# Kernel tuning notes

Hardware: AMD Instinct MI355X
Metric: run time of the kernel (lower is better)

The kernel has to match this reference:

```python
import math
import jax, jax.numpy as jnp
import numpy as np

DEGREE = 8
N = 8388608


def setup_inputs() -> dict:
    key = jax.random.key(0)
    k1, k2 = jax.random.split(key)
    X = jax.random.normal(k1, (N,), dtype=jnp.float32)
    w = jax.random.normal(k2, (DEGREE,), dtype=jnp.float32) * 0.1
    b = jnp.zeros((1,), dtype=jnp.float32)
    return {"X": X, "w": w, "b": b}


def reference(X, w, b):
    # exponents 0..degree-1; broadcast power expansion over the batch
    exponents = jnp.arange(DEGREE, dtype=jnp.float32)              # [D]
    gamma_factors = jnp.asarray(
        [1.0 / math.gamma(i + 1) for i in range(DEGREE)], dtype=jnp.float32
    )                                                              # [D]
    poly = jnp.power(X[:, None], exponents[None, :])               # [N, D]
    poly = poly * gamma_factors                                    # [N, D]
    return poly @ w + b                                            # [N]
```

## Files before the change

### kernel.cpp

```cpp
#include <hip/hip_runtime.h>
#include <hip/hip_bf16.h>


__global__ __launch_bounds__(256) void PolyModel_poly_kernel(
    const float* __restrict__ X,
    const float* __restrict__ w,
    const float* __restrict__ b,
    float* __restrict__ out,
    int n4)
{
    const float c0 = w[0] + b[0];
    const float c1 = w[1];
    const float c2 = w[2] * 0.5f;
    const float c3 = w[3] * (1.0f / 6.0f);
    const float c4 = w[4] * (1.0f / 24.0f);
    const float c5 = w[5] * (1.0f / 120.0f);
    const float c6 = w[6] * (1.0f / 720.0f);
    const float c7 = w[7] * (1.0f / 5040.0f);

    const int stride = gridDim.x * blockDim.x;
    for (int i = blockIdx.x * blockDim.x + threadIdx.x; i < n4; i += stride) {
        float4 x = reinterpret_cast<const float4*>(X)[i];
        float4 r;
        r.x = fmaf(fmaf(fmaf(fmaf(fmaf(fmaf(fmaf(c7, x.x, c6), x.x, c5), x.x, c4), x.x, c3), x.x, c2), x.x, c1), x.x, c0);
        r.y = fmaf(fmaf(fmaf(fmaf(fmaf(fmaf(fmaf(c7, x.y, c6), x.y, c5), x.y, c4), x.y, c3), x.y, c2), x.y, c1), x.y, c0);
        r.z = fmaf(fmaf(fmaf(fmaf(fmaf(fmaf(fmaf(c7, x.z, c6), x.z, c5), x.z, c4), x.z, c3), x.z, c2), x.z, c1), x.z, c0);
        r.w = fmaf(fmaf(fmaf(fmaf(fmaf(fmaf(fmaf(c7, x.w, c6), x.w, c5), x.w, c4), x.w, c3), x.w, c2), x.w, c1), x.w, c0);
        reinterpret_cast<float4*>(out)[i] = r;
    }
}

extern "C" void kernel_launch(void* const* d_in, const int* in_sizes, int n_in,
                              void* d_out, int out_size, void* d_ws, size_t ws_size,
                              hipStream_t stream) {
    const float* X = (const float*)d_in[0];
    const float* w = (const float*)d_in[1];
    const float* b = (const float*)d_in[2];
    float* out = (float*)d_out;

    const int n = in_sizes[0];
    const int n4 = n / 4;

    const int block = 256;
    int grid = (n4 + block - 1) / block;
    if (grid > 2048) grid = 2048;

    PolyModel_poly_kernel<<<grid, block, 0, stream>>>(X, w, b, out, n4);
}
```

Baseline: 15.76 us.

## Add exact-fit unrolled kernel with nontemporal loads and stores

Adds a fast-path kernel used when the size divides evenly. Each thread issues four independent float4 nontemporal loads up front, then computes and writes with nontemporal stores. The grid is sized exactly to the work instead of a capped grid-stride loop. This aims to raise memory-level parallelism, drop loop overhead and avoid polluting the cache on a streaming workload, at the cost of a second code path.

```diff
diff --git a/kernel.cpp b/kernel.cpp
--- a/kernel.cpp
+++ b/kernel.cpp
@@ -2,11 +2,62 @@
 #include <hip/hip_bf16.h>
 
 
-__global__ __launch_bounds__(256) void PolyModel_poly_kernel(
-    const float* __restrict__ X,
+typedef float f32x4 __attribute__((ext_vector_type(4)));
+
+#define UNROLL 4
+
+__device__ __forceinline__ float horner8(float x, float c0, float c1, float c2,
+                                         float c3, float c4, float c5, float c6,
+                                         float c7) {
+    float r = fmaf(c7, x, c6);
+    r = fmaf(r, x, c5);
+    r = fmaf(r, x, c4);
+    r = fmaf(r, x, c3);
+    r = fmaf(r, x, c2);
+    r = fmaf(r, x, c1);
+    r = fmaf(r, x, c0);
+    return r;
+}
+
+__global__ __launch_bounds__(256) void PolyModel_poly_fast(
+    const f32x4* __restrict__ X,
     const float* __restrict__ w,
     const float* __restrict__ b,
-    float* __restrict__ out,
+    f32x4* __restrict__ out,
+    int stride)
+{
+    const float c0 = w[0] + b[0];
+    const float c1 = w[1];
+    const float c2 = w[2] * 0.5f;
+    const float c3 = w[3] * (1.0f / 6.0f);
+    const float c4 = w[4] * (1.0f / 24.0f);
+    const float c5 = w[5] * (1.0f / 120.0f);
+    const float c6 = w[6] * (1.0f / 720.0f);
+    const float c7 = w[7] * (1.0f / 5040.0f);
+
+    const int tid = blockIdx.x * blockDim.x + threadIdx.x;
+
+    f32x4 x[UNROLL];
+#pragma unroll
+    for (int u = 0; u < UNROLL; ++u)
+        x[u] = __builtin_nontemporal_load(&X[tid + u * stride]);
+
+#pragma unroll
+    for (int u = 0; u < UNROLL; ++u) {
+        f32x4 r;
+        r.x = horner8(x[u].x, c0, c1, c2, c3, c4, c5, c6, c7);
+        r.y = horner8(x[u].y, c0, c1, c2, c3, c4, c5, c6, c7);
+        r.z = horner8(x[u].z, c0, c1, c2, c3, c4, c5, c6, c7);
+        r.w = horner8(x[u].w, c0, c1, c2, c3, c4, c5, c6, c7);
+        __builtin_nontemporal_store(r, &out[tid + u * stride]);
+    }
+}
+
+__global__ __launch_bounds__(256) void PolyModel_poly_generic(
+    const f32x4* __restrict__ X,
+    const float* __restrict__ w,
+    const float* __restrict__ b,
+    f32x4* __restrict__ out,
     int n4)
 {
     const float c0 = w[0] + b[0];
@@ -20,30 +71,36 @@
 
     const int stride = gridDim.x * blockDim.x;
     for (int i = blockIdx.x * blockDim.x + threadIdx.x; i < n4; i += stride) {
-        float4 x = reinterpret_cast<const float4*>(X)[i];
-        float4 r;
-        r.x = fmaf(fmaf(fmaf(fmaf(fmaf(fmaf(fmaf(c7, x.x, c6), x.x, c5), x.x, c4), x.x, c3), x.x, c2), x.x, c1), x.x, c0);
-        r.y = fmaf(fmaf(fmaf(fmaf(fmaf(fmaf(fmaf(c7, x.y, c6), x.y, c5), x.y, c4), x.y, c3), x.y, c2), x.y, c1), x.y, c0);
-        r.z = fmaf(fmaf(fmaf(fmaf(fmaf(fmaf(fmaf(c7, x.z, c6), x.z, c5), x.z, c4), x.z, c3), x.z, c2), x.z, c1), x.z, c0);
-        r.w = fmaf(fmaf(fmaf(fmaf(fmaf(fmaf(fmaf(c7, x.w, c6), x.w, c5), x.w, c4), x.w, c3), x.w, c2), x.w, c1), x.w, c0);
-        reinterpret_cast<float4*>(out)[i] = r;
+        f32x4 x = X[i];
+        f32x4 r;
+        r.x = horner8(x.x, c0, c1, c2, c3, c4, c5, c6, c7);
+        r.y = horner8(x.y, c0, c1, c2, c3, c4, c5, c6, c7);
+        r.z = horner8(x.z, c0, c1, c2, c3, c4, c5, c6, c7);
+        r.w = horner8(x.w, c0, c1, c2, c3, c4, c5, c6, c7);
+        out[i] = r;
     }
 }
 
 extern "C" void kernel_launch(void* const* d_in, const int* in_sizes, int n_in,
                               void* d_out, int out_size, void* d_ws, size_t ws_size,
                               hipStream_t stream) {
-    const float* X = (const float*)d_in[0];
+    const f32x4* X = (const f32x4*)d_in[0];
     const float* w = (const float*)d_in[1];
     const float* b = (const float*)d_in[2];
-    float* out = (float*)d_out;
+    f32x4* out = (f32x4*)d_out;
 
     const int n = in_sizes[0];
     const int n4 = n / 4;
 
     const int block = 256;
-    int grid = (n4 + block - 1) / block;
-    if (grid > 2048) grid = 2048;
+    const int threads_needed = n4 / UNROLL;
 
-    PolyModel_poly_kernel<<<grid, block, 0, stream>>>(X, w, b, out, n4);
+    if ((n % 4 == 0) && (n4 % (block * UNROLL) == 0)) {
+        const int grid = threads_needed / block;
+        PolyModel_poly_fast<<<grid, block, 0, stream>>>(X, w, b, out, threads_needed);
+    } else {
+        int grid = (n4 + block - 1) / block;
+        if (grid > 2048) grid = 2048;
+        PolyModel_poly_generic<<<grid, block, 0, stream>>>(X, w, b, out, n4);
+    }
 }
```

New measurement: 15.99 us. No clear change (+1.4%).
